# Kernel tuning notes

Measured on AMD Instinct MI355X. Metric: run time of the kernel, lower is better.

Reference implementation:

```python
import jax, jax.numpy as jnp
import numpy as np

MEMORY_SIZE = 100000
FEATURE_DIM = 1024
BATCH = 4096


def setup_inputs() -> dict:
    key = jax.random.key(0)
    k1, k2, k3 = jax.random.split(key, 3)
    return {
        "features": jax.random.normal(k1, (BATCH, FEATURE_DIM), dtype=jnp.float32),
        "predictions": jax.random.normal(k2, (BATCH, FEATURE_DIM), dtype=jnp.float32),
        "confidences": jax.random.uniform(k3, (BATCH,), dtype=jnp.float32),
        "memory_features": jnp.zeros((MEMORY_SIZE, FEATURE_DIM), dtype=jnp.float32),
        "memory_predictions": jnp.zeros((MEMORY_SIZE, FEATURE_DIM), dtype=jnp.float32),
        "memory_confidences": jnp.ones((MEMORY_SIZE,), dtype=jnp.float32),
        "memory_index": 12345,
        "memory_full": 0,
    }


def reference(features, predictions, confidences,
              memory_features, memory_predictions, memory_confidences,
              memory_index, memory_full):
    # Vectorized equivalent of the per-sample circular-buffer write loop.
    M, D = memory_features.shape
    B = features.shape[0]
    # Slots written by the loop: (memory_index + i) % M for i in range(B).
    # B <= M so all indices are unique and .at[].set matches sequential writes.
    idx = (memory_index + jnp.arange(B)) % M  # [B]
    new_feat = memory_features.at[idx].set(features)
    new_pred = memory_predictions.at[idx].set(predictions)
    new_conf = memory_confidences.at[idx].set(confidences)
    new_index = (memory_index + B) % M
    wrapped = (memory_index + B) >= M  # loop hit memory_index == 0 at least once
    full = jnp.logical_or(jnp.asarray(memory_full, dtype=bool), jnp.asarray(wrapped))
    utilization = jnp.where(full, jnp.float32(1.0),
                            jnp.float32(new_index) / jnp.float32(M))
    conf_mean = confidences.mean()
    return new_feat, new_pred, new_conf, conf_mean, utilization
```

## Files before the change

kernel.cpp:

```cpp
#include <hip/hip_runtime.h>

typedef float f32x4 __attribute__((ext_vector_type(4)));

__global__ __launch_bounds__(256)
void fused_update(const f32x4* __restrict__ memf,
                  const f32x4* __restrict__ memp,
                  const f32x4* __restrict__ batf,
                  const f32x4* __restrict__ batp,
                  f32x4* __restrict__ outf,
                  f32x4* __restrict__ outp,
                  const float* __restrict__ memc,
                  const float* __restrict__ batc,
                  float* __restrict__ outc,
                  const int* __restrict__ d_mi,
                  int M, int B, int D4, int shift, int total4) {
    const int mi = *d_mi;
    const int stride = gridDim.x * blockDim.x;
    const int tid0 = blockIdx.x * blockDim.x + threadIdx.x;

    for (int c = tid0; c < M; c += stride) {
        int rel = c - mi; if (rel < 0) rel += M;
        const float* src = (rel < B) ? (batc + rel) : (memc + c);
        __builtin_nontemporal_store(__builtin_nontemporal_load(src), outc + c);
    }

    const int mask = D4 - 1;

#define BODY(G)                                                              \
    {                                                                        \
        int g_ = (G);                                                        \
        int row_, off_;                                                      \
        if (shift >= 0) { row_ = g_ >> shift; off_ = g_ & mask; }            \
        else            { row_ = g_ / D4;     off_ = g_ - row_ * D4; }       \
        int rel_ = row_ - mi; if (rel_ < 0) rel_ += M;                       \
        int s_ = rel_ * D4 + off_;                                           \
        const f32x4* sf_ = (rel_ < B) ? (batf + s_) : (memf + g_);           \
        const f32x4* sp_ = (rel_ < B) ? (batp + s_) : (memp + g_);           \
        f32x4 vf_ = __builtin_nontemporal_load(sf_);                         \
        f32x4 vp_ = __builtin_nontemporal_load(sp_);                         \
        __builtin_nontemporal_store(vf_, outf + g_);                         \
        __builtin_nontemporal_store(vp_, outp + g_);                         \
    }

    int g = tid0;
    for (; g + stride < total4; g += 2 * stride) {
        BODY(g)
        BODY(g + stride)
    }
    if (g < total4) BODY(g)
#undef BODY
}

__global__ void mean_and_util(const float* __restrict__ conf,
                              const int* __restrict__ d_mi,
                              const int* __restrict__ d_full,
                              float* __restrict__ out_mean,
                              float* __restrict__ out_util,
                              int B, int M) {
    __shared__ float warp_sums[8];
    float s = 0.0f;
    for (int i = threadIdx.x; i < B; i += blockDim.x) s += conf[i];
    #pragma unroll
    for (int off = 32; off > 0; off >>= 1) s += __shfl_down(s, off);
    int lane = threadIdx.x & 63;
    int wave = threadIdx.x >> 6;
    if (lane == 0) warp_sums[wave] = s;
    __syncthreads();
    if (threadIdx.x == 0) {
        int nwaves = (blockDim.x + 63) >> 6;
        float total = 0.0f;
        for (int w = 0; w < nwaves; ++w) total += warp_sums[w];
        out_mean[0] = total / (float)B;

        int mi = *d_mi;
        int ni = (mi + B) % M;
        bool wrapped = (mi + B) >= M;
        bool full = (*d_full != 0) || wrapped;
        out_util[0] = full ? 1.0f : (float)ni / (float)M;
    }
}

extern "C" void kernel_launch(void* const* d_in, const int* in_sizes, int n_in,
                              void* d_out, int out_size, void* d_ws, size_t ws_size,
                              hipStream_t stream) {
    const float* features     = (const float*)d_in[0];
    const float* predictions  = (const float*)d_in[1];
    const float* confidences  = (const float*)d_in[2];
    const float* mem_feat     = (const float*)d_in[3];
    const float* mem_pred     = (const float*)d_in[4];
    const float* mem_conf     = (const float*)d_in[5];
    const int*   d_mi         = (const int*)d_in[6];
    const int*   d_full       = (const int*)d_in[7];

    const int B  = in_sizes[2];
    const int MD = in_sizes[3];
    const int M  = in_sizes[5];
    const int D  = MD / M;
    const int D4 = D / 4;
    const int total4 = M * D4;
    const int shift  = ((D4 & (D4 - 1)) == 0) ? __builtin_ctz(D4) : -1;

    float* out       = (float*)d_out;
    float* out_feat  = out;
    float* out_pred  = out + (size_t)MD;
    float* out_conf  = out + (size_t)2 * MD;
    float* out_mean  = out_conf + M;
    float* out_util  = out_mean + 1;

    const int blocks = 2048;

    fused_update<<<blocks, 256, 0, stream>>>(
        (const f32x4*)mem_feat, (const f32x4*)mem_pred,
        (const f32x4*)features, (const f32x4*)predictions,
        (f32x4*)out_feat, (f32x4*)out_pred,
        mem_conf, confidences, out_conf,
        d_mi, M, B, D4, shift, total4);

    mean_and_util<<<1, 256, 0, stream>>>(confidences, d_mi, d_full,
                                         out_mean, out_util, B, M);
}
```

Before: 1.291 ms.

## Map one block per row and drop nontemporal loads and stores

Restructures the copy kernel so each block handles whole rows, with the thread index as the column in float4 units. Row selection and the batch-or-memory decision are computed once per row instead of per element. Switches from nontemporal to ordinary loads and stores and removes the shift/divide indexing. Block size now equals D/4 (256 here), so the kernel assumes D/4 fits in one block, and regular stores may pollute the cache.

New measurement: 1.360 ms. +5.3%, slower.

```diff
diff --git a/kernel.cpp b/kernel.cpp
--- a/kernel.cpp
+++ b/kernel.cpp
@@ -13,42 +13,47 @@
                   const float* __restrict__ batc,
                   float* __restrict__ outc,
                   const int* __restrict__ d_mi,
-                  int M, int B, int D4, int shift, int total4) {
-    const int mi = *d_mi;
-    const int stride = gridDim.x * blockDim.x;
-    const int tid0 = blockIdx.x * blockDim.x + threadIdx.x;
+                  int M, int B, int D4) {
+    const int mi  = *d_mi;
+    const int tid = threadIdx.x;
 
-    for (int c = tid0; c < M; c += stride) {
+    for (int c = blockIdx.x * blockDim.x + tid; c < M; c += gridDim.x * blockDim.x) {
         int rel = c - mi; if (rel < 0) rel += M;
-        const float* src = (rel < B) ? (batc + rel) : (memc + c);
-        __builtin_nontemporal_store(__builtin_nontemporal_load(src), outc + c);
+        outc[c] = (rel < B) ? batc[rel] : memc[c];
     }
 
-    const int mask = D4 - 1;
+    const int rstride = gridDim.x;
 
-#define BODY(G)                                                              \
-    {                                                                        \
-        int g_ = (G);                                                        \
-        int row_, off_;                                                      \
-        if (shift >= 0) { row_ = g_ >> shift; off_ = g_ & mask; }            \
-        else            { row_ = g_ / D4;     off_ = g_ - row_ * D4; }       \
-        int rel_ = row_ - mi; if (rel_ < 0) rel_ += M;                       \
-        int s_ = rel_ * D4 + off_;                                           \
-        const f32x4* sf_ = (rel_ < B) ? (batf + s_) : (memf + g_);           \
-        const f32x4* sp_ = (rel_ < B) ? (batp + s_) : (memp + g_);           \
-        f32x4 vf_ = __builtin_nontemporal_load(sf_);                         \
-        f32x4 vp_ = __builtin_nontemporal_load(sp_);                         \
-        __builtin_nontemporal_store(vf_, outf + g_);                         \
-        __builtin_nontemporal_store(vp_, outp + g_);                         \
+#define ROW_ADDRS(R, SF, SP, DST)                                            \
+    int rel##R = (R) - mi; if (rel##R < 0) rel##R += M;                      \
+    size_t DST = (size_t)(R) * D4 + tid;                                     \
+    const f32x4* SF; const f32x4* SP;                                        \
+    if (rel##R < B) { size_t s = (size_t)rel##R * D4 + tid;                  \
+                      SF = batf + s; SP = batp + s; }                        \
+    else            { SF = memf + DST; SP = memp + DST; }
+
+    int row = blockIdx.x;
+    for (; row + rstride < M; row += 2 * rstride) {
+        int r1 = row + rstride;
+        ROW_ADDRS(row, sf0, sp0, d0)
+        ROW_ADDRS(r1,  sf1, sp1, d1)
+        f32x4 a = *sf0;
+        f32x4 b = *sp0;
+        f32x4 c = *sf1;
+        f32x4 d = *sp1;
+        outf[d0] = a;
+        outp[d0] = b;
+        outf[d1] = c;
+        outp[d1] = d;
     }
-
-    int g = tid0;
-    for (; g + stride < total4; g += 2 * stride) {
-        BODY(g)
-        BODY(g + stride)
+    if (row < M) {
+        ROW_ADDRS(row, sf0, sp0, d0)
+        f32x4 a = *sf0;
+        f32x4 b = *sp0;
+        outf[d0] = a;
+        outp[d0] = b;
     }
-    if (g < total4) BODY(g)
-#undef BODY
+#undef ROW_ADDRS
 }
 
 __global__ void mean_and_util(const float* __restrict__ conf,
@@ -97,8 +102,6 @@
     const int M  = in_sizes[5];
     const int D  = MD / M;
     const int D4 = D / 4;
-    const int total4 = M * D4;
-    const int shift  = ((D4 & (D4 - 1)) == 0) ? __builtin_ctz(D4) : -1;
 
     float* out       = (float*)d_out;
     float* out_feat  = out;
@@ -109,12 +112,12 @@
 
     const int blocks = 2048;
 
-    fused_update<<<blocks, 256, 0, stream>>>(
+    fused_update<<<blocks, D4, 0, stream>>>(
         (const f32x4*)mem_feat, (const f32x4*)mem_pred,
         (const f32x4*)features, (const f32x4*)predictions,
         (f32x4*)out_feat, (f32x4*)out_pred,
         mem_conf, confidences, out_conf,
-        d_mi, M, B, D4, shift, total4);
+        d_mi, M, B, D4);
 
     mean_and_util<<<1, 256, 0, stream>>>(confidences, d_mi, d_full,
                                          out_mean, out_util, B, M);
```
